# Kernel optimization log

Hardware: AMD Instinct MI355X
Metric: run time of the kernel (lower is better)

Reference implementation:

```python
import jax, jax.numpy as jnp
import numpy as np
from jax import lax

T = 16          # timesteps
EPS = 1e-12     # torch F.normalize eps
DN = ('NCHW', 'OIHW', 'NCHW')

def conv2d(x, w, pad):
    return lax.conv_general_dilated(x, w, (1, 1), [(pad, pad), (pad, pad)],
                                    dimension_numbers=DN)

def setup_inputs() -> dict:
    key = jax.random.key(0)
    ks = jax.random.split(key, 7)
    B, C, H, W, K = 16, 512, 14, 14, 64
    return {
        'input_tensor': jax.random.normal(ks[0], (B * T, C, H, W), jnp.float32),
        'centers': jax.random.normal(ks[1], (K, C), jnp.float32) * 0.05,
        'share_w': jax.random.normal(ks[2], (K, C, 1, 1), jnp.float32) * 0.05,
        'share_b': jax.random.uniform(ks[3], (K,), jnp.float32),
        'U_z': jax.random.normal(ks[4], (K, K, 3, 3), jnp.float32) * 0.05,
        'U_r': jax.random.normal(ks[5], (K, K, 3, 3), jnp.float32) * 0.05,
        'U_h': jax.random.normal(ks[6], (K, K, 3, 3), jnp.float32) * 0.05,
    }

def reference(input_tensor, centers, share_w, share_b, U_z, U_r, U_h):
    NT, C, H, W = input_tensor.shape
    B = NT // T
    K = centers.shape[0]

    # soft-assignment pre-activation: 1x1 conv (SAME) -> [B*T, K, H, W]
    wxb = conv2d(input_tensor, share_w, 0) + share_b[None, :, None, None]
    wxb = wxb.reshape(B, T, K, H, W).transpose(1, 0, 2, 3, 4)  # [T,B,K,H,W]

    def gru_step(h, wxb_t):
        z = jax.nn.sigmoid(wxb_t + conv2d(h, U_z, 1))
        r = jax.nn.sigmoid(wxb_t + conv2d(h, U_r, 1))
        hh = jnp.tanh(wxb_t + conv2d(r * h, U_h, 1))
        h_new = (1.0 - z) * hh + z * h
        return h_new, h_new

    h0 = jnp.zeros((B, K, H, W), input_tensor.dtype)
    _, assign = lax.scan(gru_step, h0, wxb)            # [T,B,K,H,W]
    assign = assign.transpose(1, 0, 2, 3, 4).reshape(B * T, K, H * W)

    a_sum = assign.sum(-1, keepdims=True)              # [BT,K,1]
    a = a_sum * centers[None]                          # [BT,K,C]
    feats = input_tensor.reshape(B * T, C, H * W)
    x = jnp.einsum('nks,ncs->nkc', assign, feats)      # [BT,K,C]

    vlad = (x - a).reshape(B, T, K, C).sum(1)          # [B,K,C]
    vlad = vlad / jnp.maximum(jnp.linalg.norm(vlad, axis=2, keepdims=True), EPS)
    vlad = vlad.reshape(B, K * C)
    vlad = vlad / jnp.maximum(jnp.linalg.norm(vlad, axis=1, keepdims=True), EPS)
    return vlad
```

## Files before the change

### kernel.cpp

```cpp
#include <hip/hip_runtime.h>

#define Bc 16
#define Tc 16
#define Cc 512
#define Kc 64
#define Sc 196
#define KS (Kc*Sc)
#define BKS (Bc*Kc*Sc)
#define TBKS (Tc*BKS)
#define GFIN (16*64*512)
#define PART_N (8*GFIN)
#define PX 256
#define PLB2 (Kc*PX)

__device__ __forceinline__ float sigmoid_f(float x) { return 1.f / (1.f + __expf(-x)); }
__device__ __forceinline__ float tanh_f(float x) { return 1.f - 2.f / (__expf(2.f * x) + 1.f); }

__device__ __forceinline__ float b2f(unsigned short u) {
    return __uint_as_float(((unsigned)u) << 16);
}
__device__ __forceinline__ unsigned short f2b(float f) {
    unsigned u = __float_as_uint(f);
    return (unsigned short)((u + 0x7FFFu + ((u >> 16) & 1u)) >> 16);
}

__device__ __forceinline__ float dpp_prev(float v) {
    return __int_as_float(__builtin_amdgcn_mov_dpp(__float_as_int(v), 0x111, 0xf, 0xf, true));
}
__device__ __forceinline__ float dpp_next(float v) {
    return __int_as_float(__builtin_amdgcn_mov_dpp(__float_as_int(v), 0x101, 0xf, 0xf, true));
}

__global__ __launch_bounds__(256) void k_transpose_w(const float* __restrict__ w, float* __restrict__ wt) {
    int idx = blockIdx.x * 256 + threadIdx.x;
    if (idx < Kc * Cc) {
        int k = idx & 63, c = idx >> 6;
        wt[idx] = w[k * Cc + c];
    }
}

__global__ __launch_bounds__(256) void k_conv1x1(const float* __restrict__ x, const float* __restrict__ wt,
                                                 const float* __restrict__ bias, float* __restrict__ wxb) {
    __shared__ float Xs[64][64];
    const int tid = threadIdx.x;
    const int gs0 = blockIdx.x * 64;
    const int kw = __builtin_amdgcn_readfirstlane((tid >> 6) << 4);
    const int lane = tid & 63;
    const int rbase = (tid >> 6) * 16;
    const int gs_c = gs0 + lane;
    const int n_c = gs_c / Sc, s_c = gs_c - n_c * Sc;
    const float* xcol = x + (size_t)n_c * (Cc * Sc) + s_c;

    float xr[16];
#pragma unroll
    for (int q = 0; q < 16; ++q) xr[q] = xcol[(size_t)(rbase + q) * Sc];
    float acc[16] = {};
    for (int c0 = 0; c0 < Cc; c0 += 64) {
        __syncthreads();
#pragma unroll
        for (int q = 0; q < 16; ++q) Xs[rbase + q][lane] = xr[q];
        __syncthreads();
        if (c0 + 64 < Cc) {
#pragma unroll
            for (int q = 0; q < 16; ++q) xr[q] = xcol[(size_t)(c0 + 64 + rbase + q) * Sc];
        }
#pragma unroll 8
        for (int cc = 0; cc < 64; ++cc) {
            const float xv = Xs[cc][lane];
            const float* wp = wt + (size_t)(c0 + cc) * Kc + kw;
#pragma unroll
            for (int i = 0; i < 16; ++i) acc[i] += wp[i] * xv;
        }
    }
    const int t = n_c & 15, bb = n_c >> 4;
    float* op = wxb + (((size_t)t * Bc + bb) * Kc + kw) * Sc + s_c;
#pragma unroll
    for (int i = 0; i < 16; ++i)
        op[(size_t)i * Sc] = acc[i] + bias[kw + i];
}

__global__ __launch_bounds__(64) void k_gru_t0(const float* __restrict__ wxb,
        float* __restrict__ hplane32, unsigned short* __restrict__ hplane16,
        unsigned short* __restrict__ rhplane16, float* __restrict__ assign) {
    const int blk = blockIdx.x;
    const size_t pbase = (size_t)blk * PX;
    const size_t cbase = (size_t)blk * Sc;
    for (int i = threadIdx.x; i < PX; i += 64) {
        int row = i >> 4, col = i & 15;
        float v = 0.f;
        if (row >= 1 && row <= 14 && col >= 1 && col <= 14) {
            int s = (row - 1) * 14 + (col - 1);
            float pre = wxb[cbase + s];
            v = (1.f - sigmoid_f(pre)) * tanh_f(pre);
            assign[cbase + s] = v;
        }
        hplane32[pbase + i] = v;
        hplane16[pbase + i] = f2b(v);
        rhplane16[pbase + i] = 0;
    }
}

__global__ __launch_bounds__(512) void k_gru_gates(const unsigned short* __restrict__ hplane16,
        const float* __restrict__ wxb_t, const float* __restrict__ Uz, const float* __restrict__ Ur,
        float* __restrict__ zb, unsigned short* __restrict__ rhplane16) {
    extern __shared__ float lds[];
    unsigned short* P = (unsigned short*)lds;
    float* red = lds + 8192;
    const int b = blockIdx.x;
    const int k0 = blockIdx.y * 4;
    const int tid = threadIdx.x;
    const int wv = __builtin_amdgcn_readfirstlane(tid >> 6);
    const int lane = tid & 63;
    const int kp = wv >> 2, kiq = wv & 3;

    float preE[4]; bool valE[4]; size_t csE[4]; int kEa[4];
#pragma unroll
    for (int q = 0; q < 4; ++q) {
        const int o = tid + q * 512;
        const int set = o >> 8, px = o & 255;
        const int kp_o = set >> 2, r = set & 1;
        kEa[q] = k0 + kp_o * 2 + r;
        const int row = px >> 4, col = px & 15;
        valE[q] = (row >= 1 && row <= 14 && col >= 1 && col <= 14);
        csE[q] = ((size_t)b * Kc + kEa[q]) * Sc + (valE[q] ? (row - 1) * 14 + (col - 1) : 0);
        preE[q] = valE[q] ? wxb_t[csE[q]] : 0.f;
    }
    {
        const float4* src = (const float4*)(hplane16 + (size_t)b * PLB2);
        float4* dst = (float4*)P;
#pragma unroll
        for (int it = 0; it < 4; ++it) dst[it * 512 + tid] = src[it * 512 + tid];
    }
    __syncthreads();

    const int yp = lane >> 2, xq = (lane & 3) << 2;
    const int rowbase = (yp > 0) ? (yp - 1) : 0;
    const float* uz0 = Uz + (size_t)(k0 + kp * 2) * 576 + kiq * 144;
    const float* ur0 = Ur + (size_t)(k0 + kp * 2) * 576 + kiq * 144;
    float az[2][4] = {}, ar[2][4] = {};
    const unsigned short* Pw = P + (size_t)(kiq * 16) * PX + rowbase * 16 + xq;
#pragma unroll 2
    for (int ki = 0; ki < 16; ++ki) {
        const unsigned short* pk = Pw + ki * PX;
#pragma unroll
        for (int dy = 0; dy < 3; ++dy) {
            ushort4 u = *(const ushort4*)(pk + dy * 16);
            float4 m = make_float4(b2f(u.x), b2f(u.y), b2f(u.z), b2f(u.w));
            float e0 = dpp_prev(m.w);
            float e4 = dpp_next(m.x);
#pragma unroll
            for (int r = 0; r < 2; ++r) {
                const float* wz = uz0 + r * 576 + ki * 9 + dy * 3;
                float c0 = wz[0], c1 = wz[1], c2 = wz[2];
                az[r][0] += c0*e0  + c1*m.x + c2*m.y;
                az[r][1] += c0*m.x + c1*m.y + c2*m.z;
                az[r][2] += c0*m.y + c1*m.z + c2*m.w;
                az[r][3] += c0*m.z + c1*m.w + c2*e4;
                const float* wr = ur0 + r * 576 + ki * 9 + dy * 3;
                float d0 = wr[0], d1 = wr[1], d2 = wr[2];
                ar[r][0] += d0*e0  + d1*m.x + d2*m.y;
                ar[r][1] += d0*m.x + d1*m.y + d2*m.z;
                ar[r][2] += d0*m.y + d1*m.z + d2*m.w;
                ar[r][3] += d0*m.z + d1*m.w + d2*e4;
            }
        }
    }
    {
        float* rp = red + (size_t)wv * 1024 + lane;
#pragma unroll
        for (int r = 0; r < 2; ++r)
#pragma unroll
            for (int jj = 0; jj < 4; ++jj) {
                rp[(size_t)(r * 4 + jj) * 64] = az[r][jj];
                rp[(size_t)(8 + r * 4 + jj) * 64] = ar[r][jj];
            }
    }
    __syncthreads();
#pragma unroll
    for (int q = 0; q < 4; ++q) {
        const int o = tid + q * 512;
        const int set = o >> 8, px = o & 255;
        const int kp_o = set >> 2, g = (set >> 1) & 1, r = set & 1;
        const int lane_r = ((px >> 4) << 2) + ((px & 15) >> 2);
        const int v = (g * 2 + r) * 4 + (px & 3);
        float s0 = 0.f;
#pragma unroll
        for (int kq2 = 0; kq2 < 4; ++kq2)
            s0 += red[(size_t)((kp_o * 4 + kq2) * 16 + v) * 64 + lane_r];
        if (valE[q]) {
            float sv = sigmoid_f(preE[q] + s0);
            if (g == 0) {
                zb[csE[q]] = sv;
            } else {
                float hv = b2f(P[(size_t)kEa[q] * PX + px]);
                rhplane16[(size_t)b * PLB2 + (size_t)kEa[q] * PX + px] = f2b(sv * hv);
            }
        }
    }
}

__global__ __launch_bounds__(512) void k_gru_out(const unsigned short* __restrict__ rhplane16,
        const float* __restrict__ wxb_t, const float* __restrict__ Uh, const float* __restrict__ zb,
        float* __restrict__ hplane32, unsigned short* __restrict__ hplane16,
        float* __restrict__ assign_t) {
    extern __shared__ float lds[];
    unsigned short* P = (unsigned short*)lds;
    float* red = lds + 8192;
    const int b = blockIdx.x;
    const int k0 = blockIdx.y * 4;
    const int tid = threadIdx.x;
    const int wv = __builtin_amdgcn_readfirstlane(tid >> 6);
    const int lane = tid & 63;
    const int kp = wv >> 2, kiq = wv & 3;

    float preE[2], zvE[2], hpE[2]; bool valE[2]; size_t csE[2], ppE[2];
#pragma unroll
    for (int q = 0; q < 2; ++q) {
        const int o = tid + q * 512;
        const int set = o >> 8, px = o & 255;
        const int kp_o = set >> 1, r = set & 1;
        const int k = k0 + kp_o * 2 + r;
        const int row = px >> 4, col = px & 15;
        valE[q] = (row >= 1 && row <= 14 && col >= 1 && col <= 14);
        csE[q] = ((size_t)b * Kc + k) * Sc + (valE[q] ? (row - 1) * 14 + (col - 1) : 0);
        ppE[q] = (size_t)b * PLB2 + (size_t)k * PX + px;
        preE[q] = 0.f; zvE[q] = 0.f; hpE[q] = 0.f;
        if (valE[q]) {
            preE[q] = wxb_t[csE[q]];
            zvE[q] = zb[csE[q]];
            hpE[q] = hplane32[ppE[q]];
        }
    }
    {
        const float4* src = (const float4*)(rhplane16 + (size_t)b * PLB2);
        float4* dst = (float4*)P;
#pragma unroll
        for (int it = 0; it < 4; ++it) dst[it * 512 + tid] = src[it * 512 + tid];
    }
    __syncthreads();

    const int yp = lane >> 2, xq = (lane & 3) << 2;
    const int rowbase = (yp > 0) ? (yp - 1) : 0;
    const float* uh0 = Uh + (size_t)(k0 + kp * 2) * 576 + kiq * 144;
    float ah[2][4] = {};
    const unsigned short* Pw = P + (size_t)(kiq * 16) * PX + rowbase * 16 + xq;
#pragma unroll 2
    for (int ki = 0; ki < 16; ++ki) {
        const unsigned short* pk = Pw + ki * PX;
#pragma unroll
        for (int dy = 0; dy < 3; ++dy) {
            ushort4 u = *(const ushort4*)(pk + dy * 16);
            float4 m = make_float4(b2f(u.x), b2f(u.y), b2f(u.z), b2f(u.w));
            float e0 = dpp_prev(m.w);
            float e4 = dpp_next(m.x);
#pragma unroll
            for (int r = 0; r < 2; ++r) {
                const float* wh = uh0 + r * 576 + ki * 9 + dy * 3;
                float c0 = wh[0], c1 = wh[1], c2 = wh[2];
                ah[r][0] += c0*e0  + c1*m.x + c2*m.y;
                ah[r][1] += c0*m.x + c1*m.y + c2*m.z;
                ah[r][2] += c0*m.y + c1*m.z + c2*m.w;
                ah[r][3] += c0*m.z + c1*m.w + c2*e4;
            }
        }
    }
    {
        float* rp = red + (size_t)wv * 512 + lane;
#pragma unroll
        for (int r = 0; r < 2; ++r)
#pragma unroll
            for (int jj = 0; jj < 4; ++jj)
                rp[(size_t)(r * 4 + jj) * 64] = ah[r][jj];
    }
    __syncthreads();
#pragma unroll
    for (int q = 0; q < 2; ++q) {
        const int o = tid + q * 512;
        const int set = o >> 8, px = o & 255;
        const int kp_o = set >> 1, r = set & 1;
        const int lane_r = ((px >> 4) << 2) + ((px & 15) >> 2);
        const int v = r * 4 + (px & 3);
        float s0 = 0.f;
#pragma unroll
        for (int kq2 = 0; kq2 < 4; ++kq2)
            s0 += red[(size_t)((kp_o * 4 + kq2) * 8 + v) * 64 + lane_r];
        if (valE[q]) {
            float hh = tanh_f(preE[q] + s0);
            float hn = (1.f - zvE[q]) * hh + zvE[q] * hpE[q];
            hplane32[ppE[q]] = hn;
            hplane16[ppE[q]] = f2b(hn);
            assign_t[csE[q]] = hn;
        }
    }
}

__global__ __launch_bounds__(256) void k_einsum(const float* __restrict__ x, const float* __restrict__ assign,
                                                float* __restrict__ part) {
    extern __shared__ float lds[];
    float* As = lds;
    float* Xs = lds + 196 * 68;
    const int ch = blockIdx.x, tg = blockIdx.y, b = blockIdx.z;
    const int tid = threadIdx.x;
    const int w = tid >> 6, lane = tid & 63;
    const int kt3 = lane >> 3, ct3 = lane & 7;
    const int kbase = kt3 * 8;
    const int cbase = w * 32 + ct3 * 4;
    float4 acc[8] = {};
    for (int tt = 0; tt < 2; ++tt) {
        const int t = tg * 2 + tt;
        const int n = b * Tc + t;
        __syncthreads();
        {
            const float* ap = assign + ((size_t)t * Bc + b) * KS;
            for (int q = tid; q < 3136; q += 256) {
                int kq = q / Sc, s = q - kq * Sc;
                int k4 = kq * 4;
                float4 v;
                v.x = ap[(size_t)(k4 + 0) * Sc + s];
                v.y = ap[(size_t)(k4 + 1) * Sc + s];
                v.z = ap[(size_t)(k4 + 2) * Sc + s];
                v.w = ap[(size_t)(k4 + 3) * Sc + s];
                *(float4*)(As + (size_t)s * 68 + k4) = v;
            }
        }
        for (int sc = 0; sc < 7; ++sc) {
            const int sb = sc * 28;
            __syncthreads();
            {
                const int c = tid & 127, sh = tid >> 7;
                const float* xp = x + ((size_t)n * Cc + ch * 128 + c) * Sc + sb + sh * 16;
                const int nf = sh ? 3 : 4;
                for (int f = 0; f < nf; ++f) {
                    float4 v = *(const float4*)(xp + f * 4);
                    float* dst = Xs + (size_t)(sh * 16 + f * 4) * 132 + c;
                    dst[0] = v.x; dst[132] = v.y; dst[264] = v.z; dst[396] = v.w;
                }
            }
            __syncthreads();
#pragma unroll 4
            for (int s = 0; s < 28; ++s) {
                const float* ap = As + (size_t)(sb + s) * 68 + kbase;
                float4 a0 = *(const float4*)ap;
                float4 a1 = *(const float4*)(ap + 4);
                float4 xv = *(const float4*)(Xs + (size_t)s * 132 + cbase);
                float av[8] = {a0.x,a0.y,a0.z,a0.w,a1.x,a1.y,a1.z,a1.w};
#pragma unroll
                for (int i = 0; i < 8; ++i) {
                    acc[i].x += av[i] * xv.x;
                    acc[i].y += av[i] * xv.y;
                    acc[i].z += av[i] * xv.z;
                    acc[i].w += av[i] * xv.w;
                }
            }
        }
    }
#pragma unroll
    for (int i = 0; i < 8; ++i) {
        const int k = kbase + i;
        float* op = part + (((size_t)tg * Bc + b) * Kc + k) * Cc + ch * 128 + cbase;
        *(float4*)op = acc[i];
    }
}

__global__ __launch_bounds__(256) void k_reduce(const float* __restrict__ assign, const float* __restrict__ part,
        const float* __restrict__ centers, float* __restrict__ vlad, float* __restrict__ norm2) {
    __shared__ float redw[4];
    __shared__ float a_s;
    const int blk = blockIdx.x;
    const int b = blk >> 6, k = blk & 63;
    const int tid = threadIdx.x;
    const int wave = tid >> 6, lane = tid & 63;
    const size_t bkoff = ((size_t)b * Kc + k) * Sc;
    float s = 0.f;
    for (int q = tid; q < 784; q += 256) {
        int t = q / 49, s4 = q - t * 49;
        float4 v = *(const float4*)(assign + (size_t)t * BKS + bkoff + s4 * 4);
        s += (v.x + v.y) + (v.z + v.w);
    }
#pragma unroll
    for (int o = 1; o < 64; o <<= 1) s += __shfl_xor(s, o);
    if (lane == 0) redw[wave] = s;
    __syncthreads();
    if (tid == 0) a_s = redw[0] + redw[1] + redw[2] + redw[3];
    __syncthreads();
    const float a = a_s;
    const size_t base = ((size_t)b * Kc + k) * Cc;
    const int c = tid * 2;
    float2 acc2 = make_float2(0.f, 0.f);
#pragma unroll
    for (int g = 0; g < 8; ++g) {
        float2 p = *(const float2*)(part + (size_t)g * GFIN + base + c);
        acc2.x += p.x; acc2.y += p.y;
    }
    float2 cv = *(const float2*)(centers + (size_t)k * Cc + c);
    float v0 = acc2.x - a * cv.x, v1 = acc2.y - a * cv.y;
    *(float2*)(vlad + base + c) = make_float2(v0, v1);
    float ss = v0 * v0 + v1 * v1;
#pragma unroll
    for (int o = 1; o < 64; o <<= 1) ss += __shfl_xor(ss, o);
    __syncthreads();
    if (lane == 0) redw[wave] = ss;
    __syncthreads();
    if (tid == 0) norm2[blk] = redw[0] + redw[1] + redw[2] + redw[3];
}

__global__ __launch_bounds__(64) void k_norms(const float* __restrict__ norm2, float* __restrict__ scl) {
    const int b = blockIdx.x;
    const int k = threadIdx.x;
    float ss = norm2[b * Kc + k];
    float inv = 1.f / fmaxf(sqrtf(ss), 1e-12f);
    float g = ss * inv * inv;
#pragma unroll
    for (int o = 1; o < 64; o <<= 1) g += __shfl_xor(g, o);
    float gi = 1.f / fmaxf(sqrtf(g), 1e-12f);
    scl[b * Kc + k] = inv * gi;
}

__global__ __launch_bounds__(256) void k_scale(const float* __restrict__ vlad, const float* __restrict__ scl,
                                               float* __restrict__ out) {
    const int blk = blockIdx.x;
    const int b = blk >> 4, kt = blk & 15;
    const int tid = threadIdx.x;
    const int kk = tid >> 6, lane = tid & 63;
    const int k = kt * 4 + kk;
    const float sv = scl[b * Kc + k];
    const float* vp = vlad + ((size_t)b * Kc + k) * Cc + lane * 8;
    float* op = out + ((size_t)b * Kc + k) * Cc + lane * 8;
    float4 v0 = *(const float4*)vp;
    float4 v1 = *(const float4*)(vp + 4);
    *(float4*)op = make_float4(v0.x * sv, v0.y * sv, v0.z * sv, v0.w * sv);
    *(float4*)(op + 4) = make_float4(v1.x * sv, v1.y * sv, v1.z * sv, v1.w * sv);
}

extern "C" void kernel_launch(void* const* d_in, const int* in_sizes, int n_in,
                              void* d_out, int out_size, void* d_ws, size_t ws_size,
                              hipStream_t stream) {
    (void)in_sizes; (void)n_in; (void)out_size; (void)ws_size;
    const float* x       = (const float*)d_in[0];
    const float* centers = (const float*)d_in[1];
    const float* share_w = (const float*)d_in[2];
    const float* share_b = (const float*)d_in[3];
    const float* Uz      = (const float*)d_in[4];
    const float* Ur      = (const float*)d_in[5];
    const float* Uh      = (const float*)d_in[6];
    float* out = (float*)d_out;
    float* ws  = (float*)d_ws;

    float* part      = ws;
    float* vlad      = ws;
    float* wxb       = ws;
    unsigned short* rhplane16 = (unsigned short*)(ws + (size_t)TBKS);
    unsigned short* hplane16  = (unsigned short*)(ws + (size_t)TBKS + 131072);
    float* assign   = ws + (size_t)PART_N;
    float* zb       = assign + (size_t)TBKS;
    float* hplane32 = zb + (size_t)BKS;
    float* wt       = hplane32 + (size_t)Bc * PLB2;
    float* norm2    = wt + (size_t)Kc * Cc;
    float* scl      = norm2 + (size_t)Bc * Kc;

    const size_t gates_lds = 65536;
    const size_t outk_lds  = 49152;
    const size_t ein_lds   = (size_t)(196 * 68 + 28 * 132) * 4;

    k_transpose_w<<<dim3(128), 256, 0, stream>>>(share_w, wt);
    k_conv1x1<<<dim3(784), 256, 0, stream>>>(x, wt, share_b, wxb);
    k_gru_t0<<<dim3(1024), 64, 0, stream>>>(wxb, hplane32, hplane16, rhplane16, assign);
    for (int t = 1; t < Tc; ++t) {
        k_gru_gates<<<dim3(16, 16), 512, gates_lds, stream>>>(hplane16, wxb + (size_t)t * BKS,
                                                              Uz, Ur, zb, rhplane16);
        k_gru_out<<<dim3(16, 16), 512, outk_lds, stream>>>(rhplane16, wxb + (size_t)t * BKS,
                                                           Uh, zb, hplane32, hplane16,
                                                           assign + (size_t)t * BKS);
    }
    k_einsum<<<dim3(4, 8, 16), 256, ein_lds, stream>>>(x, assign, part);
    k_reduce<<<dim3(Bc * Kc), 256, 0, stream>>>(assign, part, centers, vlad, norm2);
    k_norms<<<dim3(Bc), 64, 0, stream>>>(norm2, scl);
    k_scale<<<dim3(256), 256, 0, stream>>>(vlad, scl, out);
}
```

Baseline: 459.3 us.

## Move 1x1 conv and einsum to split-bf16 MFMA matrix cores

```diff
diff --git a/kernel.cpp b/kernel.cpp
--- a/kernel.cpp
+++ b/kernel.cpp
@@ -13,6 +13,9 @@
 #define PX 256
 #define PLB2 (Kc*PX)
 
+typedef __attribute__((ext_vector_type(8))) short bf16x8;
+typedef __attribute__((ext_vector_type(4))) float f32x4;
+
 __device__ __forceinline__ float sigmoid_f(float x) { return 1.f / (1.f + __expf(-x)); }
 __device__ __forceinline__ float tanh_f(float x) { return 1.f - 2.f / (__expf(2.f * x) + 1.f); }
 
@@ -23,6 +26,13 @@
     unsigned u = __float_as_uint(f);
     return (unsigned short)((u + 0x7FFFu + ((u >> 16) & 1u)) >> 16);
 }
+__device__ __forceinline__ void split1(float f, unsigned short& h, unsigned short& l) {
+    unsigned u = __float_as_uint(f);
+    unsigned uh = u & 0xffff0000u;
+    h = (unsigned short)(uh >> 16);
+    float fl = f - __uint_as_float(uh);
+    l = (unsigned short)(__float_as_uint(fl) >> 16);
+}
 
 __device__ __forceinline__ float dpp_prev(float v) {
     return __int_as_float(__builtin_amdgcn_mov_dpp(__float_as_int(v), 0x111, 0xf, 0xf, true));
@@ -31,52 +41,66 @@
     return __int_as_float(__builtin_amdgcn_mov_dpp(__float_as_int(v), 0x101, 0xf, 0xf, true));
 }
 
-__global__ __launch_bounds__(256) void k_transpose_w(const float* __restrict__ w, float* __restrict__ wt) {
+__global__ __launch_bounds__(256) void k_prep_w(const float* __restrict__ w,
+        unsigned short* __restrict__ wh, unsigned short* __restrict__ wl) {
     int idx = blockIdx.x * 256 + threadIdx.x;
-    if (idx < Kc * Cc) {
-        int k = idx & 63, c = idx >> 6;
-        wt[idx] = w[k * Cc + c];
-    }
-}
-
-__global__ __launch_bounds__(256) void k_conv1x1(const float* __restrict__ x, const float* __restrict__ wt,
-                                                 const float* __restrict__ bias, float* __restrict__ wxb) {
-    __shared__ float Xs[64][64];
+    unsigned short h, l;
+    split1(w[idx], h, l);
+    wh[idx] = h; wl[idx] = l;
+}
+
+__global__ __launch_bounds__(512) void k_conv1x1(const float* __restrict__ x,
+        const unsigned short* __restrict__ wh, const unsigned short* __restrict__ wl,
+        const float* __restrict__ bias, float* __restrict__ wxb) {
+    extern __shared__ float lds[];
+    unsigned short* Xh = (unsigned short*)lds;
+    unsigned short* Xl = Xh + 64 * 40;
+    const int gs0 = blockIdx.x * 64;
     const int tid = threadIdx.x;
-    const int gs0 = blockIdx.x * 64;
-    const int kw = __builtin_amdgcn_readfirstlane((tid >> 6) << 4);
-    const int lane = tid & 63;
-    const int rbase = (tid >> 6) * 16;
-    const int gs_c = gs0 + lane;
-    const int n_c = gs_c / Sc, s_c = gs_c - n_c * Sc;
-    const float* xcol = x + (size_t)n_c * (Cc * Sc) + s_c;
-
-    float xr[16];
-#pragma unroll
-    for (int q = 0; q < 16; ++q) xr[q] = xcol[(size_t)(rbase + q) * Sc];
-    float acc[16] = {};
-    for (int c0 = 0; c0 < Cc; c0 += 64) {
+    const int wv = tid >> 6, lane = tid & 63;
+    const int lg = lane >> 4, ln = lane & 15;
+    const int mt = wv & 3, np = wv >> 2;
+    const int colS = tid & 63, cgS = tid >> 6;
+    const int gsS = gs0 + colS;
+    const int nS = gsS / Sc, sS = gsS - nS * Sc;
+    const float* xcol = x + (size_t)nS * (Cc * Sc) + sS;
+    const int kA = np * 32 + ln;
+    const float bias0 = bias[kA], bias1 = bias[kA + 16];
+
+    f32x4 acc0 = {0.f, 0.f, 0.f, 0.f}, acc1 = {0.f, 0.f, 0.f, 0.f};
+    for (int c0 = 0; c0 < Cc; c0 += 32) {
         __syncthreads();
 #pragma unroll
-        for (int q = 0; q < 16; ++q) Xs[rbase + q][lane] = xr[q];
+        for (int q = 0; q < 4; ++q) {
+            const int cl = cgS * 4 + q;
+            unsigned short h, l;
+            split1(xcol[(size_t)(c0 + cl) * Sc], h, l);
+            Xh[colS * 40 + cl] = h;
+            Xl[colS * 40 + cl] = l;
+        }
         __syncthreads();
-        if (c0 + 64 < Cc) {
-#pragma unroll
-            for (int q = 0; q < 16; ++q) xr[q] = xcol[(size_t)(c0 + 64 + rbase + q) * Sc];
-        }
-#pragma unroll 8
-        for (int cc = 0; cc < 64; ++cc) {
-            const float xv = Xs[cc][lane];
-            const float* wp = wt + (size_t)(c0 + cc) * Kc + kw;
-#pragma unroll
-            for (int i = 0; i < 16; ++i) acc[i] += wp[i] * xv;
-        }
-    }
-    const int t = n_c & 15, bb = n_c >> 4;
-    float* op = wxb + (((size_t)t * Bc + bb) * Kc + kw) * Sc + s_c;
-#pragma unroll
-    for (int i = 0; i < 16; ++i)
-        op[(size_t)i * Sc] = acc[i] + bias[kw + i];
+        bf16x8 B0h = *(const bf16x8*)(wh + (size_t)kA * Cc + c0 + lg * 8);
+        bf16x8 B0l = *(const bf16x8*)(wl + (size_t)kA * Cc + c0 + lg * 8);
+        bf16x8 B1h = *(const bf16x8*)(wh + (size_t)(kA + 16) * Cc + c0 + lg * 8);
+        bf16x8 B1l = *(const bf16x8*)(wl + (size_t)(kA + 16) * Cc + c0 + lg * 8);
+        bf16x8 Af = *(const bf16x8*)(Xh + (mt * 16 + ln) * 40 + lg * 8);
+        bf16x8 Al = *(const bf16x8*)(Xl + (mt * 16 + ln) * 40 + lg * 8);
+        acc0 = __builtin_amdgcn_mfma_f32_16x16x32_bf16(Af, B0h, acc0, 0, 0, 0);
+        acc0 = __builtin_amdgcn_mfma_f32_16x16x32_bf16(Al, B0h, acc0, 0, 0, 0);
+        acc0 = __builtin_amdgcn_mfma_f32_16x16x32_bf16(Af, B0l, acc0, 0, 0, 0);
+        acc1 = __builtin_amdgcn_mfma_f32_16x16x32_bf16(Af, B1h, acc1, 0, 0, 0);
+        acc1 = __builtin_amdgcn_mfma_f32_16x16x32_bf16(Al, B1h, acc1, 0, 0, 0);
+        acc1 = __builtin_amdgcn_mfma_f32_16x16x32_bf16(Af, B1l, acc1, 0, 0, 0);
+    }
+#pragma unroll
+    for (int r = 0; r < 4; ++r) {
+        const int gs = gs0 + mt * 16 + lg * 4 + r;
+        const int n = gs / Sc, s = gs - (gs / Sc) * Sc;
+        const int t = n & 15, bb = n >> 4;
+        const size_t rowbase = ((size_t)t * Bc + bb) * Kc;
+        wxb[(rowbase + kA) * Sc + s] = acc0[r] + bias0;
+        wxb[(rowbase + kA + 16) * Sc + s] = acc1[r] + bias1;
+    }
 }
 
 __global__ __launch_bounds__(64) void k_gru_t0(const float* __restrict__ wxb,
@@ -294,71 +318,73 @@
     }
 }
 
-__global__ __launch_bounds__(256) void k_einsum(const float* __restrict__ x, const float* __restrict__ assign,
+__global__ __launch_bounds__(512) void k_einsum(const float* __restrict__ x, const float* __restrict__ assign,
                                                 float* __restrict__ part) {
     extern __shared__ float lds[];
-    float* As = lds;
-    float* Xs = lds + 196 * 68;
-    const int ch = blockIdx.x, tg = blockIdx.y, b = blockIdx.z;
+    unsigned short* Ah = (unsigned short*)lds;
+    unsigned short* Al = Ah + 64 * 40;
+    unsigned short* Xh = Al + 64 * 40;
+    unsigned short* Xl = Xh + 128 * 40;
+    const int cq = blockIdx.x, tg = blockIdx.y, b = blockIdx.z;
     const int tid = threadIdx.x;
-    const int w = tid >> 6, lane = tid & 63;
-    const int kt3 = lane >> 3, ct3 = lane & 7;
-    const int kbase = kt3 * 8;
-    const int cbase = w * 32 + ct3 * 4;
-    float4 acc[8] = {};
+    const int wv = tid >> 6, lane = tid & 63;
+    const int lg = lane >> 4, ln = lane & 15;
+    const int ka = tid >> 3, ss4 = (tid & 7) * 4;
+    const int cx = tid >> 2, ss8 = (tid & 3) * 8;
+
+    f32x4 acc[4];
+#pragma unroll
+    for (int mt = 0; mt < 4; ++mt) acc[mt] = (f32x4){0.f, 0.f, 0.f, 0.f};
+
     for (int tt = 0; tt < 2; ++tt) {
         const int t = tg * 2 + tt;
         const int n = b * Tc + t;
-        __syncthreads();
-        {
-            const float* ap = assign + ((size_t)t * Bc + b) * KS;
-            for (int q = tid; q < 3136; q += 256) {
-                int kq = q / Sc, s = q - kq * Sc;
-                int k4 = kq * 4;
-                float4 v;
-                v.x = ap[(size_t)(k4 + 0) * Sc + s];
-                v.y = ap[(size_t)(k4 + 1) * Sc + s];
-                v.z = ap[(size_t)(k4 + 2) * Sc + s];
-                v.w = ap[(size_t)(k4 + 3) * Sc + s];
-                *(float4*)(As + (size_t)s * 68 + k4) = v;
-            }
-        }
-        for (int sc = 0; sc < 7; ++sc) {
-            const int sb = sc * 28;
+        const float* ap = assign + ((size_t)t * Bc + b) * KS;
+        const float* xp = x + ((size_t)n * Cc + cq * 128) * Sc;
+        for (int sc7 = 0; sc7 < 7; ++sc7) {
+            const int s0 = sc7 * 32;
             __syncthreads();
             {
-                const int c = tid & 127, sh = tid >> 7;
-                const float* xp = x + ((size_t)n * Cc + ch * 128 + c) * Sc + sb + sh * 16;
-                const int nf = sh ? 3 : 4;
-                for (int f = 0; f < nf; ++f) {
-                    float4 v = *(const float4*)(xp + f * 4);
-                    float* dst = Xs + (size_t)(sh * 16 + f * 4) * 132 + c;
-                    dst[0] = v.x; dst[132] = v.y; dst[264] = v.z; dst[396] = v.w;
-                }
+                float4 v = make_float4(0.f, 0.f, 0.f, 0.f);
+                if (s0 + ss4 <= 192) v = *(const float4*)(ap + (size_t)ka * Sc + s0 + ss4);
+                ushort4 h, l;
+                split1(v.x, h.x, l.x); split1(v.y, h.y, l.y);
+                split1(v.z, h.z, l.z); split1(v.w, h.w, l.w);
+                *(ushort4*)(Ah + ka * 40 + ss4) = h;
+                *(ushort4*)(Al + ka * 40 + ss4) = l;
+            }
+#pragma unroll
+            for (int q = 0; q < 2; ++q) {
+                const int so = ss8 + q * 4;
+                float4 v = make_float4(0.f, 0.f, 0.f, 0.f);
+                if (s0 + so <= 192) v = *(const float4*)(xp + (size_t)cx * Sc + s0 + so);
+                ushort4 h, l;
+                split1(v.x, h.x, l.x); split1(v.y, h.y, l.y);
+                split1(v.z, h.z, l.z); split1(v.w, h.w, l.w);
+                *(ushort4*)(Xh + cx * 40 + so) = h;
+                *(ushort4*)(Xl + cx * 40 + so) = l;
             }
             __syncthreads();
-#pragma unroll 4
-            for (int s = 0; s < 28; ++s) {
-                const float* ap = As + (size_t)(sb + s) * 68 + kbase;
-                float4 a0 = *(const float4*)ap;
-                float4 a1 = *(const float4*)(ap + 4);
-                float4 xv = *(const float4*)(Xs + (size_t)s * 132 + cbase);
-                float av[8] = {a0.x,a0.y,a0.z,a0.w,a1.x,a1.y,a1.z,a1.w};
-#pragma unroll
-                for (int i = 0; i < 8; ++i) {
-                    acc[i].x += av[i] * xv.x;
-                    acc[i].y += av[i] * xv.y;
-                    acc[i].z += av[i] * xv.z;
-                    acc[i].w += av[i] * xv.w;
-                }
-            }
-        }
-    }
-#pragma unroll
-    for (int i = 0; i < 8; ++i) {
-        const int k = kbase + i;
-        float* op = part + (((size_t)tg * Bc + b) * Kc + k) * Cc + ch * 128 + cbase;
-        *(float4*)op = acc[i];
+            bf16x8 Bh = *(const bf16x8*)(Xh + (wv * 16 + ln) * 40 + lg * 8);
+            bf16x8 Bl = *(const bf16x8*)(Xl + (wv * 16 + ln) * 40 + lg * 8);
+#pragma unroll
+            for (int mt = 0; mt < 4; ++mt) {
+                bf16x8 Af = *(const bf16x8*)(Ah + (mt * 16 + ln) * 40 + lg * 8);
+                bf16x8 Alo = *(const bf16x8*)(Al + (mt * 16 + ln) * 40 + lg * 8);
+                acc[mt] = __builtin_amdgcn_mfma_f32_16x16x32_bf16(Af, Bh, acc[mt], 0, 0, 0);
+                acc[mt] = __builtin_amdgcn_mfma_f32_16x16x32_bf16(Alo, Bh, acc[mt], 0, 0, 0);
+                acc[mt] = __builtin_amdgcn_mfma_f32_16x16x32_bf16(Af, Bl, acc[mt], 0, 0, 0);
+            }
+        }
+    }
+    const int c = cq * 128 + wv * 16 + ln;
+#pragma unroll
+    for (int mt = 0; mt < 4; ++mt) {
+#pragma unroll
+        for (int r = 0; r < 4; ++r) {
+            const int k = mt * 16 + lg * 4 + r;
+            part[(((size_t)tg * Bc + b) * Kc + k) * Cc + c] = acc[mt][r];
+        }
     }
 }
 
@@ -454,16 +480,19 @@
     float* assign   = ws + (size_t)PART_N;
     float* zb       = assign + (size_t)TBKS;
     float* hplane32 = zb + (size_t)BKS;
-    float* wt       = hplane32 + (size_t)Bc * PLB2;
-    float* norm2    = wt + (size_t)Kc * Cc;
+    float* wreg     = hplane32 + (size_t)Bc * PLB2;
+    unsigned short* w_hi = (unsigned short*)wreg;
+    unsigned short* w_lo = w_hi + (size_t)Kc * Cc;
+    float* norm2    = wreg + (size_t)Kc * Cc;
     float* scl      = norm2 + (size_t)Bc * Kc;
 
+    const size_t conv_lds  = 64 * 40 * 2 * 2;
     const size_t gates_lds = 65536;
     const size_t outk_lds  = 49152;
-    const size_t ein_lds   = (size_t)(196 * 68 + 28 * 132) * 4;
-
-    k_transpose_w<<<dim3(128), 256, 0, stream>>>(share_w, wt);
-    k_conv1x1<<<dim3(784), 256, 0, stream>>>(x, wt, share_b, wxb);
+    const size_t ein_lds   = (64 * 40 + 128 * 40) * 2 * 2;
+
+    k_prep_w<<<dim3(128), 256, 0, stream>>>(share_w, w_hi, w_lo);
+    k_conv1x1<<<dim3(784), 512, conv_lds, stream>>>(x, w_hi, w_lo, share_b, wxb);
     k_gru_t0<<<dim3(1024), 64, 0, stream>>>(wxb, hplane32, hplane16, rhplane16, assign);
     for (int t = 1; t < Tc; ++t) {
         k_gru_gates<<<dim3(16, 16), 512, gates_lds, stream>>>(hplane16, wxb + (size_t)t * BKS,
@@ -472,7 +501,7 @@
                                                            Uh, zb, hplane32, hplane16,
                                                            assign + (size_t)t * BKS);
     }
-    k_einsum<<<dim3(4, 8, 16), 256, ein_lds, stream>>>(x, assign, part);
+    k_einsum<<<dim3(4, 8, 16), 512, ein_lds, stream>>>(x, assign, part);
     k_reduce<<<dim3(Bc * Kc), 256, 0, stream>>>(assign, part, centers, vlad, norm2);
     k_norms<<<dim3(Bc), 64, 0, stream>>>(norm2, scl);
     k_scale<<<dim3(256), 256, 0, stream>>>(vlad, scl, out);
```

Result: no change. 455.0 us (-0.9%).
